# Optimization experiments

Measured on AMD Instinct MI355X. Metric: run time of the kernel, lower is better.

## Reference

```python
import jax, jax.numpy as jnp
import numpy as np

V, E, H, T = 100000, 128, 256, 7
B, S = 64, 512
START, STOP = 5, 6
H2 = H // 2


def setup_inputs() -> dict:
    key = jax.random.key(0)
    ks = jax.random.split(key, 16)
    rn = lambda k, shape, s=0.1: jax.random.normal(k, shape, jnp.float32) * s
    inp = {}
    inp["sentence"] = jax.random.randint(ks[0], (B, S), 0, V)
    inp["tags"] = jax.random.randint(ks[1], (B, S), 0, 5)
    inp["h0"] = jax.random.normal(ks[2], (2, B, H2), jnp.float32)
    inp["c0"] = jax.random.normal(ks[3], (2, B, H2), jnp.float32)
    inp["embedding"] = rn(ks[4], (V, E), 1.0)
    inp["w_ih_f"] = rn(ks[5], (4 * H2, E)); inp["w_hh_f"] = rn(ks[6], (4 * H2, H2))
    inp["b_ih_f"] = rn(ks[7], (4 * H2,)); inp["b_hh_f"] = rn(ks[8], (4 * H2,))
    inp["w_ih_b"] = rn(ks[9], (4 * H2, E)); inp["w_hh_b"] = rn(ks[10], (4 * H2, H2))
    inp["b_ih_b"] = rn(ks[11], (4 * H2,)); inp["b_hh_b"] = rn(ks[12], (4 * H2,))
    inp["w_out"] = rn(ks[13], (T, H)); inp["b_out"] = rn(ks[14], (T,))
    trans = jax.random.normal(ks[15], (T, T), jnp.float32)
    trans = trans.at[START, :].set(-10000.0).at[:, STOP].set(-10000.0)
    inp["transitions"] = trans
    return inp


def _lstm_dir(x, h0, c0, wih, whh, bih, bhh, reverse):
    # x: [S, B, E]; PyTorch gate order i, f, g, o
    def step(carry, xt):
        h, c = carry
        z = xt @ wih.T + h @ whh.T + bih + bhh  # [B, 4*H2]
        i, f, g, o = jnp.split(z, 4, axis=-1)
        c = jax.nn.sigmoid(f) * c + jax.nn.sigmoid(i) * jnp.tanh(g)
        h = jax.nn.sigmoid(o) * jnp.tanh(c)
        return (h, c), h
    _, hs = jax.lax.scan(step, (h0, c0), x, reverse=reverse)
    return hs  # [S, B, H2]


def reference(sentence, tags, h0, c0, embedding, w_ih_f, w_hh_f, b_ih_f, b_hh_f,
              w_ih_b, w_hh_b, b_ih_b, b_hh_b, w_out, b_out, transitions):
    # Embedding; torch code does .view(S, B, -1) on a [B, S, E] tensor (raw
    # reinterpretation) -- replicate with reshape to match the math exactly.
    embeds = embedding[sentence].reshape(S, B, E)
    hf = _lstm_dir(embeds, h0[0], c0[0], w_ih_f, w_hh_f, b_ih_f, b_hh_f, False)
    hb = _lstm_dir(embeds, h0[1], c0[1], w_ih_b, w_hh_b, b_ih_b, b_hh_b, True)
    feats = jnp.concatenate([hf, hb], axis=-1) @ w_out.T + b_out  # [S, B, T]

    # CRF forward algorithm. Original uses transitions.t(), i.e. step score
    # for prev=i -> next=j is transitions[i, j].
    alpha0 = jnp.full((B, T), -10000.0, jnp.float32).at[:, START].set(0.0)
    def crf_step(alpha, feat):
        # [b, i, j]: alpha[b,i] + transitions[i,j]; LSE over i, add emit[b,j]
        a = jax.nn.logsumexp(alpha[:, :, None] + transitions[None, :, :], axis=1) + feat
        return a, None
    alpha, _ = jax.lax.scan(crf_step, alpha0, feats)
    fwd_score = jax.nn.logsumexp(alpha + transitions[STOP][None, :], axis=1)  # [B]

    # Gold path score: transitions[next, prev] + emit[next], per _score_sentence.
    tags_ext = jnp.concatenate([jnp.full((B, 1), START, tags.dtype), tags], axis=1)
    t_prev, t_next = tags_ext[:, :-1], tags_ext[:, 1:]  # [B, S]
    trans_sc = transitions[t_next, t_prev].sum(axis=1)
    emit_sc = jnp.take_along_axis(jnp.transpose(feats, (1, 0, 2)),
                                  t_next[:, :, None], axis=2)[..., 0].sum(axis=1)
    gold = trans_sc + emit_sc + transitions[STOP, tags_ext[:, -1]]
    return jnp.sum(fwd_score - gold) / B
```

## Files before the change

### kernel.cpp

```cpp
#include <hip/hip_runtime.h>

typedef unsigned int u32;
typedef unsigned short u16;
typedef __attribute__((ext_vector_type(8))) short short8;
typedef __attribute__((ext_vector_type(4))) float f32x4;

#define DEV __device__ __forceinline__
#define LOG2E 1.44269504089f

DEV u16 f2bf(float f) {
    u32 u = __float_as_uint(f);
    return (u16)((u + 0x7FFFu + ((u >> 16) & 1u)) >> 16);
}
DEV float bf2f(u16 h) { return __uint_as_float(((u32)h) << 16); }
DEV float frcp(float x) { return __builtin_amdgcn_rcpf(x); }
DEV float fexp2(float x) {
#if __has_builtin(__builtin_amdgcn_exp2f)
    return __builtin_amdgcn_exp2f(x);
#else
    return exp2f(x);
#endif
}
DEV u32 pack_bf16(float a, float b) {
#if __has_builtin(__builtin_amdgcn_cvt_pk_bf16_f32)
    auto v = __builtin_amdgcn_cvt_pk_bf16_f32(a, b);
    u32 r; __builtin_memcpy(&r, &v, 4); return r;
#else
    return (u32)f2bf(a) | ((u32)f2bf(b) << 16);
#endif
}
DEV float xex(uint2 v, int r) {
    u32 u = (r & 2) ? v.y : v.x;
    return (r & 1) ? __uint_as_float(u & 0xFFFF0000u) : __uint_as_float(u << 16);
}

__global__ __launch_bounds__(512) void k_inproj2(
    const int* __restrict__ sent, const float* __restrict__ emb,
    const float* __restrict__ wihf, const float* __restrict__ bihf, const float* __restrict__ bhhf,
    const float* __restrict__ wihb, const float* __restrict__ bihb, const float* __restrict__ bhhb,
    u16* __restrict__ Xf, u16* __restrict__ Xb)
{
    int blk = blockIdx.x;
    int d  = blk >> 7;
    int sc = blk & 127;
    const float* wih = d ? wihb : wihf;
    const float* bih = d ? bihb : bihf;
    const float* bhh = d ? bhhb : bhhf;
    u16* X = d ? Xb : Xf;
    int tid = threadIdx.x;
    int w = tid >> 6, lane = tid & 63;
    int rg = lane >> 4, cn = lane & 15;

    short8 afr[4][4];
    #pragma unroll
    for (int mi = 0; mi < 4; ++mi) {
        int gate = 16 * (w + 8 * mi) + cn;
        #pragma unroll
        for (int kt = 0; kt < 4; ++kt) {
            const float* p = wih + (size_t)gate * 128 + kt * 32 + rg * 8;
            float4 f0 = *(const float4*)p;
            float4 f1 = *(const float4*)(p + 4);
            union { short8 v; u32 u[4]; } sv;
            sv.u[0] = pack_bf16(f0.x, f0.y);
            sv.u[1] = pack_bf16(f0.z, f0.w);
            sv.u[2] = pack_bf16(f1.x, f1.y);
            sv.u[3] = pack_bf16(f1.z, f1.w);
            afr[mi][kt] = sv.v;
        }
    }
    float bs[4][4];
    #pragma unroll
    for (int mi = 0; mi < 4; ++mi)
        #pragma unroll
        for (int r = 0; r < 4; ++r) {
            int g = 16 * (w + 8 * mi) + 4 * rg + r;
            bs[mi][r] = bih[g] + bhh[g];
        }

    __shared__ u16 tile[2][64][136];
    #pragma unroll
    for (int stage = 0; stage < 2; ++stage) {
        if (stage) __syncthreads();
        {
            int row = tid >> 2, q = tid & 3;
            int sl = row >> 6, bb = row & 63;
            int tok = sent[(sc * 4 + stage * 2 + sl) * 64 + bb];
            const float* er = emb + (size_t)tok * 128 + q * 32;
            u16* dst = &tile[sl][bb][q * 32];
            #pragma unroll
            for (int u = 0; u < 4; ++u) {
                float4 a = *(const float4*)(er + u * 8);
                float4 c = *(const float4*)(er + u * 8 + 4);
                uint4 st;
                st.x = pack_bf16(a.x, a.y); st.y = pack_bf16(a.z, a.w);
                st.z = pack_bf16(c.x, c.y); st.w = pack_bf16(c.z, c.w);
                *(uint4*)(dst + u * 8) = st;
            }
        }
        __syncthreads();
        #pragma unroll
        for (int ss = 0; ss < 2; ++ss) {
            int s = sc * 4 + stage * 2 + ss;
            #pragma unroll
            for (int nt = 0; nt < 4; ++nt) {
                short8 bfr[4];
                #pragma unroll
                for (int kt = 0; kt < 4; ++kt)
                    bfr[kt] = *(const short8*)&tile[ss][nt * 16 + cn][kt * 32 + rg * 8];
                #pragma unroll
                for (int mi = 0; mi < 4; ++mi) {
                    f32x4 acc = {0.f, 0.f, 0.f, 0.f};
                    #pragma unroll
                    for (int kt = 0; kt < 4; ++kt)
                        acc = __builtin_amdgcn_mfma_f32_16x16x32_bf16(afr[mi][kt], bfr[kt], acc, 0, 0, 0);
                    size_t base = (((size_t)s * 4 + nt) * 32 + (w + 8 * mi)) * 256
                                + (size_t)rg * 64 + (size_t)cn * 4;
                    uint2 st;
                    st.x = pack_bf16((acc[0] + bs[mi][0]) * LOG2E, (acc[1] + bs[mi][1]) * LOG2E);
                    st.y = pack_bf16((acc[2] + bs[mi][2]) * LOG2E, (acc[3] + bs[mi][3]) * LOG2E);
                    *(uint2*)(X + base) = st;
                }
            }
        }
    }
}

__global__ __launch_bounds__(512) void k_lstm(
    const float* __restrict__ h0, const float* __restrict__ c0,
    const float* __restrict__ whhf, const float* __restrict__ whhb,
    const u16* __restrict__ Xf, const u16* __restrict__ Xb,
    u16* __restrict__ hfo, u16* __restrict__ hbo)
{
    int d  = blockIdx.x >> 2, g4 = blockIdx.x & 3;
    const float* whh = d ? whhb : whhf;
    const u16*   X   = d ? Xb   : Xf;
    u16*         ho  = d ? hbo  : hfo;
    int w = threadIdx.x >> 6, lane = threadIdx.x & 63;
    int rg = lane >> 4, cn = lane & 15;

    short8 afr[4][4];
    #pragma unroll
    for (int mi = 0; mi < 4; ++mi) {
        int gate = 16 * (w + 8 * mi) + cn;
        #pragma unroll
        for (int kt = 0; kt < 4; ++kt) {
            const float* p = whh + (size_t)gate * 128 + kt * 32 + rg * 8;
            float4 f0 = *(const float4*)p;
            float4 f1 = *(const float4*)(p + 4);
            union { short8 v; u32 u[4]; } sv;
            sv.u[0] = pack_bf16(f0.x * LOG2E, f0.y * LOG2E);
            sv.u[1] = pack_bf16(f0.z * LOG2E, f0.w * LOG2E);
            sv.u[2] = pack_bf16(f1.x * LOG2E, f1.y * LOG2E);
            sv.u[3] = pack_bf16(f1.z * LOG2E, f1.w * LOG2E);
            afr[mi][kt] = sv.v;
        }
    }
    int b = g4 * 16 + cn;
    int chb = 16 * w + rg * 4;
    float cst[4];
    {
        float4 cv = *(const float4*)(c0 + ((size_t)d * 64 + b) * 128 + chb);
        cst[0]=cv.x; cst[1]=cv.y; cst[2]=cv.z; cst[3]=cv.w;
    }
    __shared__ u16 hbuf[2][16][136];
    {
        float4 hv = *(const float4*)(h0 + ((size_t)d * 64 + b) * 128 + chb);
        uint2 st0;
        st0.x = pack_bf16(hv.x, hv.y);
        st0.y = pack_bf16(hv.z, hv.w);
        *(uint2*)&hbuf[0][cn][chb] = st0;
    }
    __syncthreads();

    int s0 = d ? 511 : 0;
    const int sdelta = d ? -32768 : 32768;
    const ptrdiff_t hdelta = d ? -8192 : 8192;
    size_t lof = (size_t)rg * 64 + (size_t)cn * 4;

    const u16* pa[4]; const u16* pb[4];
    uint2 xA[4], xB[4];
    #pragma unroll
    for (int mi = 0; mi < 4; ++mi) {
        const u16* base = X + (((size_t)s0 * 4 + g4) * 32 + (w + 8 * mi)) * 256 + lof;
        xA[mi] = *(const uint2*)base;
        xB[mi] = *(const uint2*)(base + sdelta);
        pa[mi] = base + 2 * sdelta;
        pb[mi] = base + 3 * sdelta;
    }
    u16* hop = ho + ((size_t)s0 * 64 + b) * 128 + chb;

#define LSTM_STEP(RB, WB, XC, XP)                                            \
    do {                                                                     \
        short8 bfr[4];                                                       \
        _Pragma("unroll")                                                    \
        for (int kt = 0; kt < 4; ++kt)                                       \
            bfr[kt] = *(const short8*)&hbuf[RB][cn][kt * 32 + rg * 8];       \
        f32x4 z[4];                                                          \
        _Pragma("unroll")                                                    \
        for (int mi = 0; mi < 4; ++mi) {                                     \
            f32x4 acc;                                                       \
            acc[0] = xex(XC[mi], 0); acc[1] = xex(XC[mi], 1);                \
            acc[2] = xex(XC[mi], 2); acc[3] = xex(XC[mi], 3);                \
            _Pragma("unroll")                                                \
            for (int kt = 0; kt < 4; ++kt)                                   \
                acc = __builtin_amdgcn_mfma_f32_16x16x32_bf16(               \
                    afr[mi][kt], bfr[kt], acc, 0, 0, 0);                     \
            z[mi] = acc;                                                     \
            XC[mi] = *(const uint2*)XP[mi];                                  \
            XP[mi] += 2 * sdelta;                                            \
        }                                                                    \
        float hnew[4];                                                       \
        _Pragma("unroll")                                                    \
        for (int r = 0; r < 4; ++r) {                                        \
            float zi = z[0][r], zf = z[1][r], zg = z[2][r], zo = z[3][r];    \
            float ei = fexp2(-zi);                                           \
            float ef = fexp2(-zf);                                           \
            float eo = fexp2(-zo);                                           \
            float eg = fexp2(fminf(zg + zg, 115.f));                         \
            float A = 1.f + ei, F = 1.f + ef, G = eg + 1.f, O = 1.f + eo;    \
            float AG = A * G;                                                \
            float cc = (cst[r] * AG + (eg - 1.f) * F) * frcp(F * AG);        \
            cst[r] = cc;                                                     \
            float ec = fexp2(fminf(2.885390082f * cc, 115.f));               \
            hnew[r] = (ec - 1.f) * frcp(O * (ec + 1.f));                     \
        }                                                                    \
        uint2 st;                                                            \
        st.x = pack_bf16(hnew[0], hnew[1]);                                  \
        st.y = pack_bf16(hnew[2], hnew[3]);                                  \
        *(uint2*)&hbuf[WB][cn][chb] = st;                                    \
        *(uint2*)hop = st;                                                   \
        hop += hdelta;                                                       \
        asm volatile("s_waitcnt lgkmcnt(0)\n\ts_barrier" ::: "memory");      \
    } while (0)

    for (int it = 0; it < 256; ++it) {
        LSTM_STEP(0, 1, xA, pa);
        LSTM_STEP(1, 0, xB, pb);
    }
#undef LSTM_STEP
}

__global__ __launch_bounds__(256) void k_feats(
    const u16* __restrict__ hf, const u16* __restrict__ hb,
    const float* __restrict__ wout, const float* __restrict__ bout,
    float* __restrict__ feats)
{
    __shared__ u16 sf[32][136], sb[32][136];
    __shared__ float wo[7][260];
    __shared__ float bo[8];
    int tid = threadIdx.x;
    int pos0 = blockIdx.x * 32;
    {
        int r = tid >> 3, cc = (tid & 7) * 16;
        const uint4* pf = (const uint4*)(hf + (size_t)(pos0 + r) * 128 + cc);
        const uint4* pb = (const uint4*)(hb + (size_t)(pos0 + r) * 128 + cc);
        *(uint4*)&sf[r][cc]     = pf[0];
        *(uint4*)&sf[r][cc + 8] = pf[1];
        *(uint4*)&sb[r][cc]     = pb[0];
        *(uint4*)&sb[r][cc + 8] = pb[1];
    }
    for (int i = tid; i < 1792; i += 256) wo[i >> 8][i & 255] = wout[i];
    if (tid < 7) bo[tid] = bout[tid];
    __syncthreads();
    int pp = tid >> 3, tt = tid & 7;
    if (tt < 7) {
        float acc = bo[tt];
        #pragma unroll 4
        for (int ch = 0; ch < 128; ++ch)
            acc += bf2f(sf[pp][ch]) * wo[tt][ch]
                 + bf2f(sb[pp][ch]) * wo[tt][128 + ch];
        feats[(size_t)(pos0 + pp) * 7 + tt] = acc;
    }
}

__global__ __launch_bounds__(64) void k_crf_chunk(
    const float* __restrict__ feats, const float* __restrict__ trans,
    float* __restrict__ chunkM)
{
    int b = blockIdx.x >> 3, c = blockIdx.x & 7;
    int lane = threadIdx.x;
    int i = lane >> 3, j = lane & 7;
    __shared__ float M[8][8];
    __shared__ float fl[64][8];
    int s0 = c * 64;
    for (int idx = lane; idx < 448; idx += 64) {
        int ss = idx / 7, jj = idx - ss * 7;
        fl[ss][jj] = feats[(size_t)((s0 + ss) * 64 + b) * 7 + jj];
    }
    float tc[7];
    #pragma unroll
    for (int k = 0; k < 7; ++k) tc[k] = (j < 7) ? trans[k * 7 + j] : 0.f;
    __syncthreads();
    M[i][j] = (i < 7 && j < 7) ? (trans[i * 7 + j] + fl[0][j]) : -1e30f;
    __syncthreads();
    for (int ss = 1; ss < 64; ++ss) {
        float4 m0 = *(const float4*)&M[i][0];
        float4 m1 = *(const float4*)&M[i][4];
        float v0 = m0.x + tc[0], v1 = m0.y + tc[1], v2 = m0.z + tc[2];
        float v3 = m0.w + tc[3], v4 = m1.x + tc[4], v5 = m1.y + tc[5];
        float v6 = m1.z + tc[6];
        float mx = fmaxf(fmaxf(fmaxf(v0, v1), fmaxf(v2, v3)),
                         fmaxf(fmaxf(v4, v5), v6));
        float sm = __expf(v0 - mx) + __expf(v1 - mx) + __expf(v2 - mx)
                 + __expf(v3 - mx) + __expf(v4 - mx) + __expf(v5 - mx)
                 + __expf(v6 - mx);
        float r = mx + __logf(sm) + fl[ss][j];
        __syncthreads();
        if (i < 7 && j < 7) M[i][j] = r;
        __syncthreads();
    }
    if (i < 7 && j < 7)
        chunkM[(size_t)(b * 8 + c) * 49 + i * 7 + j] = M[i][j];
}

__global__ __launch_bounds__(512) void k_crf_final(
    const float* __restrict__ chunkM, const float* __restrict__ trans,
    const int* __restrict__ tags, const float* __restrict__ feats,
    float* __restrict__ out)
{
    int tid = threadIdx.x;
    int w = tid >> 6, lane = tid & 63;
    int k = lane >> 3, j = lane & 7;
    int b = w * 8 + k;
    bool jv = (j < 7);
    __shared__ float Tl[49];
    __shared__ float red[512];
    __shared__ float fsh[64];
    if (tid < 49) Tl[tid] = trans[tid];
    __syncthreads();

    float av = (j == 5) ? 0.f : -1e4f;
    #pragma unroll
    for (int c = 0; c < 8; ++c) {
        float a0 = __shfl(av, k * 8 + 0, 64);
        float a1 = __shfl(av, k * 8 + 1, 64);
        float a2 = __shfl(av, k * 8 + 2, 64);
        float a3 = __shfl(av, k * 8 + 3, 64);
        float a4 = __shfl(av, k * 8 + 4, 64);
        float a5 = __shfl(av, k * 8 + 5, 64);
        float a6 = __shfl(av, k * 8 + 6, 64);
        if (jv) {
            const float* Pp = chunkM + ((size_t)b * 8 + c) * 49 + j;
            float v0 = a0 + Pp[0],  v1 = a1 + Pp[7],  v2 = a2 + Pp[14];
            float v3 = a3 + Pp[21], v4 = a4 + Pp[28], v5 = a5 + Pp[35];
            float v6 = a6 + Pp[42];
            float mx = fmaxf(fmaxf(fmaxf(v0, v1), fmaxf(v2, v3)),
                             fmaxf(fmaxf(v4, v5), v6));
            float sm = __expf(v0 - mx) + __expf(v1 - mx) + __expf(v2 - mx)
                     + __expf(v3 - mx) + __expf(v4 - mx) + __expf(v5 - mx)
                     + __expf(v6 - mx);
            av = mx + __logf(sm);
        }
    }
    float u = jv ? (av + Tl[42 + j]) : -1e30f;
    float m = u;
    #pragma unroll
    for (int off = 1; off < 8; off <<= 1) m = fmaxf(m, __shfl_xor(m, off, 64));
    float e = jv ? __expf(u - m) : 0.f;
    #pragma unroll
    for (int off = 1; off < 8; off <<= 1) e += __shfl_xor(e, off, 64);
    float fwd = m + __logf(e);
    if (j == 0) fsh[b] = fwd;

    int tb = tid & 63, q = tid >> 6;
    const int* tgp = tags + (size_t)tb * 512;
    float acc = 0.f;
    int tp = (q == 0) ? 5 : tgp[q * 64 - 1];
    for (int ss = q * 64; ss < q * 64 + 64; ++ss) {
        int tn = tgp[ss];
        acc += Tl[tn * 7 + tp] + feats[(size_t)(ss * 64 + tb) * 7 + tn];
        tp = tn;
    }
    if (q == 7) acc += Tl[42 + tgp[511]];
    red[tid] = acc;
    __syncthreads();
    if (tid < 64) {
        float g = red[tid];
        #pragma unroll
        for (int qq = 1; qq < 8; ++qq) g += red[tid + 64 * qq];
        red[tid] = fsh[tid] - g;
    }
    __syncthreads();
    if (tid < 64) {
        float v = red[tid];
        #pragma unroll
        for (int off = 1; off < 64; off <<= 1) v += __shfl_xor(v, off, 64);
        if (tid == 0) out[0] = v * (1.0f / 64.0f);
    }
}

extern "C" void kernel_launch(void* const* d_in, const int* in_sizes, int n_in,
                              void* d_out, int out_size, void* d_ws, size_t ws_size,
                              hipStream_t stream) {
    const int*   sent = (const int*)d_in[0];
    const int*   tags = (const int*)d_in[1];
    const float* h0   = (const float*)d_in[2];
    const float* c0   = (const float*)d_in[3];
    const float* emb  = (const float*)d_in[4];
    const float* wihf = (const float*)d_in[5];
    const float* whhf = (const float*)d_in[6];
    const float* bihf = (const float*)d_in[7];
    const float* bhhf = (const float*)d_in[8];
    const float* wihb = (const float*)d_in[9];
    const float* whhb = (const float*)d_in[10];
    const float* bihb = (const float*)d_in[11];
    const float* bhhb = (const float*)d_in[12];
    const float* wout = (const float*)d_in[13];
    const float* bout = (const float*)d_in[14];
    const float* trn  = (const float*)d_in[15];

    char* ws = (char*)d_ws;
    u16*   Xf     = (u16*)(ws);
    u16*   Xb     = (u16*)(ws + 33554432);
    u16*   hfp    = (u16*)(ws + 67108864);
    u16*   hbp    = (u16*)(ws + 75497472);
    float* feats  = (float*)(ws + 83886080);
    float* chunkM = (float*)(ws + 84803584);

    k_inproj2<<<256, 512, 0, stream>>>(sent, emb, wihf, bihf, bhhf,
                                       wihb, bihb, bhhb, Xf, Xb);
    k_lstm<<<8, 512, 0, stream>>>(h0, c0, whhf, whhb, Xf, Xb, hfp, hbp);
    k_feats<<<1024, 256, 0, stream>>>(hfp, hbp, wout, bout, feats);
    k_crf_chunk<<<512, 64, 0, stream>>>(feats, trn, chunkM);
    k_crf_final<<<1, 512, 0, stream>>>(chunkM, trn, tags, feats, (float*)d_out);
}
```

Before: 572.6 us.

## Halve LSTM block to 4 waves, each computing two gate tiles per step

The recurrent LSTM kernel now runs with 256 threads (4 waves) instead of 512. Each wave owns two 16-channel column groups, so it holds twice the recurrent weight fragments and issues twice the MFMAs per step. Gate nonlinearities are rewritten on float2 pairs to encourage packed math. The aim is cheaper per-step barriers across fewer waves and better ILP within a wave on this latency-bound sequential loop. The cost is more serial MFMA work per wave and higher register pressure, which could lengthen each step.

```diff
diff --git a/kernel.cpp b/kernel.cpp
--- a/kernel.cpp
+++ b/kernel.cpp
@@ -4,6 +4,7 @@
 typedef unsigned short u16;
 typedef __attribute__((ext_vector_type(8))) short short8;
 typedef __attribute__((ext_vector_type(4))) float f32x4;
+typedef __attribute__((ext_vector_type(2))) float f32x2;
 
 #define DEV __device__ __forceinline__
 #define LOG2E 1.44269504089f
@@ -32,6 +33,25 @@
 DEV float xex(uint2 v, int r) {
     u32 u = (r & 2) ? v.y : v.x;
     return (r & 1) ? __uint_as_float(u & 0xFFFF0000u) : __uint_as_float(u << 16);
+}
+
+DEV f32x2 exp2p(f32x2 a) { f32x2 r; r.x = fexp2(a.x); r.y = fexp2(a.y); return r; }
+DEV f32x2 rcpp(f32x2 a)  { f32x2 r; r.x = frcp(a.x);  r.y = frcp(a.y);  return r; }
+DEV f32x2 minp(f32x2 a, float b) { f32x2 r; r.x = fminf(a.x, b); r.y = fminf(a.y, b); return r; }
+DEV f32x2 LOp(f32x4 v) { f32x2 r; r.x = v[0]; r.y = v[1]; return r; }
+DEV f32x2 HIp(f32x4 v) { f32x2 r; r.x = v[2]; r.y = v[3]; return r; }
+
+DEV f32x2 lstm_pair(f32x2 zi, f32x2 zf, f32x2 zg, f32x2 zo, f32x2* cst) {
+    f32x2 ei = exp2p(-zi);
+    f32x2 ef = exp2p(-zf);
+    f32x2 eo = exp2p(-zo);
+    f32x2 eg = exp2p(minp(zg + zg, 115.f));
+    f32x2 A = 1.f + ei, F = 1.f + ef, G = eg + 1.f, O = 1.f + eo;
+    f32x2 AG = A * G;
+    f32x2 cc = (*cst * AG + (eg - 1.f) * F) * rcpp(F * AG);
+    *cst = cc;
+    f32x2 ec = exp2p(minp(cc * 2.885390082f, 115.f));
+    return (ec - 1.f) * rcpp(O * (ec + 1.f));
 }
 
 __global__ __launch_bounds__(512) void k_inproj2(
@@ -125,7 +145,7 @@
     }
 }
 
-__global__ __launch_bounds__(512) void k_lstm(
+__global__ __launch_bounds__(256, 1) void k_lstm(
     const float* __restrict__ h0, const float* __restrict__ c0,
     const float* __restrict__ whhf, const float* __restrict__ whhb,
     const u16* __restrict__ Xf, const u16* __restrict__ Xb,
@@ -138,37 +158,39 @@
     int w = threadIdx.x >> 6, lane = threadIdx.x & 63;
     int rg = lane >> 4, cn = lane & 15;
 
-    short8 afr[4][4];
-    #pragma unroll
-    for (int mi = 0; mi < 4; ++mi) {
-        int gate = 16 * (w + 8 * mi) + cn;
-        #pragma unroll
-        for (int kt = 0; kt < 4; ++kt) {
-            const float* p = whh + (size_t)gate * 128 + kt * 32 + rg * 8;
-            float4 f0 = *(const float4*)p;
-            float4 f1 = *(const float4*)(p + 4);
-            union { short8 v; u32 u[4]; } sv;
-            sv.u[0] = pack_bf16(f0.x * LOG2E, f0.y * LOG2E);
-            sv.u[1] = pack_bf16(f0.z * LOG2E, f0.w * LOG2E);
-            sv.u[2] = pack_bf16(f1.x * LOG2E, f1.y * LOG2E);
-            sv.u[3] = pack_bf16(f1.z * LOG2E, f1.w * LOG2E);
-            afr[mi][kt] = sv.v;
-        }
-    }
+    short8 afr[2][4][4];
+    #pragma unroll
+    for (int c = 0; c < 2; ++c)
+        #pragma unroll
+        for (int t = 0; t < 4; ++t) {
+            int gate = 16 * (8 * t + 2 * w + c) + cn;
+            #pragma unroll
+            for (int kt = 0; kt < 4; ++kt) {
+                const float* p = whh + (size_t)gate * 128 + kt * 32 + rg * 8;
+                float4 f0 = *(const float4*)p;
+                float4 f1 = *(const float4*)(p + 4);
+                union { short8 v; u32 u[4]; } sv;
+                sv.u[0] = pack_bf16(f0.x * LOG2E, f0.y * LOG2E);
+                sv.u[1] = pack_bf16(f0.z * LOG2E, f0.w * LOG2E);
+                sv.u[2] = pack_bf16(f1.x * LOG2E, f1.y * LOG2E);
+                sv.u[3] = pack_bf16(f1.z * LOG2E, f1.w * LOG2E);
+                afr[c][t][kt] = sv.v;
+            }
+        }
     int b = g4 * 16 + cn;
-    int chb = 16 * w + rg * 4;
-    float cst[4];
-    {
-        float4 cv = *(const float4*)(c0 + ((size_t)d * 64 + b) * 128 + chb);
-        cst[0]=cv.x; cst[1]=cv.y; cst[2]=cv.z; cst[3]=cv.w;
-    }
+    int chb = 32 * w + 4 * rg;
+    f32x2 cst01[2], cst23[2];
     __shared__ u16 hbuf[2][16][136];
-    {
-        float4 hv = *(const float4*)(h0 + ((size_t)d * 64 + b) * 128 + chb);
+    #pragma unroll
+    for (int c = 0; c < 2; ++c) {
+        float4 cv = *(const float4*)(c0 + ((size_t)d * 64 + b) * 128 + chb + 16 * c);
+        cst01[c].x = cv.x; cst01[c].y = cv.y;
+        cst23[c].x = cv.z; cst23[c].y = cv.w;
+        float4 hv = *(const float4*)(h0 + ((size_t)d * 64 + b) * 128 + chb + 16 * c);
         uint2 st0;
         st0.x = pack_bf16(hv.x, hv.y);
         st0.y = pack_bf16(hv.z, hv.w);
-        *(uint2*)&hbuf[0][cn][chb] = st0;
+        *(uint2*)&hbuf[0][cn][chb + 16 * c] = st0;
     }
     __syncthreads();
 
@@ -178,14 +200,17 @@
     size_t lof = (size_t)rg * 64 + (size_t)cn * 4;
 
     const u16* pa[4]; const u16* pb[4];
-    uint2 xA[4], xB[4];
-    #pragma unroll
-    for (int mi = 0; mi < 4; ++mi) {
-        const u16* base = X + (((size_t)s0 * 4 + g4) * 32 + (w + 8 * mi)) * 256 + lof;
-        xA[mi] = *(const uint2*)base;
-        xB[mi] = *(const uint2*)(base + sdelta);
-        pa[mi] = base + 2 * sdelta;
-        pb[mi] = base + 3 * sdelta;
+    uint2 xA[2][4], xB[2][4];
+    #pragma unroll
+    for (int t = 0; t < 4; ++t) {
+        const u16* base = X + (((size_t)s0 * 4 + g4) * 32 + (8 * t + 2 * w)) * 256 + lof;
+        #pragma unroll
+        for (int c = 0; c < 2; ++c) {
+            xA[c][t] = *(const uint2*)(base + c * 256);
+            xB[c][t] = *(const uint2*)(base + sdelta + c * 256);
+        }
+        pa[t] = base + 2 * sdelta;
+        pb[t] = base + 3 * sdelta;
     }
     u16* hop = ho + ((size_t)s0 * 64 + b) * 128 + chb;
 
@@ -195,40 +220,35 @@
         _Pragma("unroll")                                                    \
         for (int kt = 0; kt < 4; ++kt)                                       \
             bfr[kt] = *(const short8*)&hbuf[RB][cn][kt * 32 + rg * 8];       \
-        f32x4 z[4];                                                          \
+        f32x4 z[2][4];                                                       \
         _Pragma("unroll")                                                    \
-        for (int mi = 0; mi < 4; ++mi) {                                     \
-            f32x4 acc;                                                       \
-            acc[0] = xex(XC[mi], 0); acc[1] = xex(XC[mi], 1);                \
-            acc[2] = xex(XC[mi], 2); acc[3] = xex(XC[mi], 3);                \
+        for (int c = 0; c < 2; ++c)                                          \
             _Pragma("unroll")                                                \
-            for (int kt = 0; kt < 4; ++kt)                                   \
-                acc = __builtin_amdgcn_mfma_f32_16x16x32_bf16(               \
-                    afr[mi][kt], bfr[kt], acc, 0, 0, 0);                     \
-            z[mi] = acc;                                                     \
-            XC[mi] = *(const uint2*)XP[mi];                                  \
-            XP[mi] += 2 * sdelta;                                            \
+            for (int t = 0; t < 4; ++t) {                                    \
+                f32x4 acc;                                                   \
+                acc[0] = xex(XC[c][t], 0); acc[1] = xex(XC[c][t], 1);        \
+                acc[2] = xex(XC[c][t], 2); acc[3] = xex(XC[c][t], 3);        \
+                _Pragma("unroll")                                            \
+                for (int kt = 0; kt < 4; ++kt)                               \
+                    acc = __builtin_amdgcn_mfma_f32_16x16x32_bf16(           \
+                        afr[c][t][kt], bfr[kt], acc, 0, 0, 0);               \
+                z[c][t] = acc;                                               \
+                XC[c][t] = *(const uint2*)(XP[t] + c * 256);                 \
+            }                                                                \
+        _Pragma("unroll")                                                    \
+        for (int t = 0; t < 4; ++t) XP[t] += 2 * sdelta;                     \
+        _Pragma("unroll")                                                    \
+        for (int c = 0; c < 2; ++c) {                                        \
+            f32x2 h01 = lstm_pair(LOp(z[c][0]), LOp(z[c][1]),                \
+                                  LOp(z[c][2]), LOp(z[c][3]), &cst01[c]);    \
+            f32x2 h23 = lstm_pair(HIp(z[c][0]), HIp(z[c][1]),                \
+                                  HIp(z[c][2]), HIp(z[c][3]), &cst23[c]);    \
+            uint2 st;                                                        \
+            st.x = pack_bf16(h01.x, h01.y);                                  \
+            st.y = pack_bf16(h23.x, h23.y);                                  \
+            *(uint2*)&hbuf[WB][cn][chb + 16 * c] = st;                       \
+            *(uint2*)(hop + 16 * c) = st;                                    \
         }                                                                    \
-        float hnew[4];                                                       \
-        _Pragma("unroll")                                                    \
-        for (int r = 0; r < 4; ++r) {                                        \
-            float zi = z[0][r], zf = z[1][r], zg = z[2][r], zo = z[3][r];    \
-            float ei = fexp2(-zi);                                           \
-            float ef = fexp2(-zf);                                           \
-            float eo = fexp2(-zo);                                           \
-            float eg = fexp2(fminf(zg + zg, 115.f));                         \
-            float A = 1.f + ei, F = 1.f + ef, G = eg + 1.f, O = 1.f + eo;    \
-            float AG = A * G;                                                \
-            float cc = (cst[r] * AG + (eg - 1.f) * F) * frcp(F * AG);        \
-            cst[r] = cc;                                                     \
-            float ec = fexp2(fminf(2.885390082f * cc, 115.f));               \
-            hnew[r] = (ec - 1.f) * frcp(O * (ec + 1.f));                     \
-        }                                                                    \
-        uint2 st;                                                            \
-        st.x = pack_bf16(hnew[0], hnew[1]);                                  \
-        st.y = pack_bf16(hnew[2], hnew[3]);                                  \
-        *(uint2*)&hbuf[WB][cn][chb] = st;                                    \
-        *(uint2*)hop = st;                                                   \
         hop += hdelta;                                                       \
         asm volatile("s_waitcnt lgkmcnt(0)\n\ts_barrier" ::: "memory");      \
     } while (0)
@@ -419,7 +439,7 @@
 
     k_inproj2<<<256, 512, 0, stream>>>(sent, emb, wihf, bihf, bhhf,
                                        wihb, bihb, bhhb, Xf, Xb);
-    k_lstm<<<8, 512, 0, stream>>>(h0, c0, whhf, whhb, Xf, Xb, hfp, hbp);
+    k_lstm<<<8, 256, 0, stream>>>(h0, c0, whhf, whhb, Xf, Xb, hfp, hbp);
     k_feats<<<1024, 256, 0, stream>>>(hfp, hbp, wout, bout, feats);
     k_crf_chunk<<<512, 64, 0, stream>>>(feats, trn, chunkM);
     k_crf_final<<<1, 512, 0, stream>>>(chunkM, trn, tags, feats, (float*)d_out);
```

After: 750.4 us. 1.31x slower.
